# Kernel tuning notes

Measured on AMD Instinct MI355X. Metric: run time of the kernel, lower is better.

The kernel has to match this reference:

```python
import jax, jax.numpy as jnp
import numpy as np

N = 4096          # total ensemble boxes per frame
M = 20            # MAX_MERGE_NUMS
H = 16            # MergeNet hidden_c
COND_THRES = 0.2
IOU_THRES = 0.3


def setup_inputs() -> dict:
    key = jax.random.key(0)
    ks = jax.random.split(key, 6)
    u = jax.random.uniform(ks[0], (N, 9), dtype=jnp.float32)
    # realistic lidar boxes: centers in a ~140x80x8m range, dims in [0.5, 4.5), heading in [-pi, pi)
    centers = (u[:, 0:3] - 0.5) * jnp.array([140.0, 80.0, 8.0], jnp.float32)
    dims = u[:, 3:6] * 4.0 + 0.5
    heading = (u[:, 6:7] - 0.5) * (2.0 * np.pi)
    extra = u[:, 7:9]  # extra box attrs (cols 7:9), untouched by merge
    pred_boxes = jnp.concatenate([centers, dims, heading, extra], axis=-1)
    pred_scores = jax.random.uniform(ks[1], (N,), dtype=jnp.float32)
    pred_labels = jax.random.randint(ks[2], (N,), 0, 3)
    w1 = (jax.random.normal(ks[3], (M, H), jnp.float32) / np.sqrt(M)).astype(jnp.float32)
    b1 = jnp.zeros((H,), jnp.float32)
    w2 = (jax.random.normal(ks[4], (H, H), jnp.float32) / np.sqrt(H)).astype(jnp.float32)
    b2 = jnp.zeros((H,), jnp.float32)
    w3 = (jax.random.normal(ks[5], (H, 1), jnp.float32) / np.sqrt(H)).astype(jnp.float32)
    b3 = jnp.zeros((1,), jnp.float32)
    return dict(pred_boxes=pred_boxes, pred_scores=pred_scores, pred_labels=pred_labels,
                w1=w1, b1=b1, w2=w2, b2=b2, w3=w3, b3=b3)


def _bev_aligned(b):
    # boxes3d_lidar_to_aligned_bev_boxes: swap dx/dy when |limit_period(heading)| >= pi/4
    ang = b[..., 6] - jnp.floor(b[..., 6] / np.pi + 0.5) * np.pi
    swap = jnp.abs(ang) >= (np.pi / 4)
    dx = jnp.where(swap, b[..., 4], b[..., 3])
    dy = jnp.where(swap, b[..., 3], b[..., 4])
    return jnp.stack([b[..., 0] - dx / 2, b[..., 1] - dy / 2,
                      b[..., 0] + dx / 2, b[..., 1] + dy / 2], axis=-1)


def _iou_one_many(a, b):
    # axis-aligned BEV IoU of one box a[4] vs many b[N,4]
    xmin = jnp.maximum(a[0], b[:, 0]); ymin = jnp.maximum(a[1], b[:, 1])
    xmax = jnp.minimum(a[2], b[:, 2]); ymax = jnp.minimum(a[3], b[:, 3])
    inter = jnp.maximum(xmax - xmin, 0.0) * jnp.maximum(ymax - ymin, 0.0)
    area_a = (a[2] - a[0]) * (a[3] - a[1])
    area_b = (b[:, 2] - b[:, 0]) * (b[:, 3] - b[:, 1])
    return inter / jnp.maximum(area_a + area_b - inter, 1e-6)


def _nms_merge(pred_boxes, pred_scores, pred_labels, w1, b1, w2, b2, w3, b3):
    valid = pred_scores > COND_THRES
    sort_key = jnp.where(valid, pred_scores, -jnp.inf)
    order = jnp.argsort(-sort_key)                 # descending by score; invalid sink
    boxes9 = pred_boxes[order]
    labels = pred_labels[order]
    scores = pred_scores[order]
    suppressed0 = ~valid[order]
    boxes7 = boxes9[:, :7]
    bev0 = _bev_aligned(boxes7)                    # merged boxes get suppressed, so bev is static

    def mergenet(ob):                              # ob: [M, 7] -> merged box [7]
        x = ob.T                                   # [7, M] (k is the feature axis)
        h = jax.nn.relu(x @ w1 + b1)
        h = jax.nn.relu(h @ w2 + b2)
        return (h @ w3 + b3)[:, 0]

    def step(suppressed, i):
        active = ~suppressed[i]
        same = (labels == labels[i]) & (~suppressed)
        iou = _iou_one_many(bev0[i], bev0)         # [N]
        over = (iou > IOU_THRES) & same            # includes self (iou=1)
        count = jnp.sum(over)
        rank = jnp.cumsum(over) - 1                # slot of each overlap, in score order
        tgt = jnp.where(over & (rank < M), rank, M)
        ob = jnp.zeros((M, 7), boxes7.dtype).at[tgt].set(boxes7, mode='drop')
        bi = boxes7[i]
        new_box = jnp.where(count > 1, mergenet(ob), bi)
        new_box = new_box.at[3:6].set(jnp.maximum(new_box[3:6], 1e-5))
        out_box = jnp.where(active, new_box, bi)
        return suppressed | (over & active), (out_box, active)

    _, (merged7, keep) = jax.lax.scan(step, suppressed0, jnp.arange(N))
    out_boxes = jnp.concatenate([merged7, boxes9[:, 7:9]], axis=-1)   # [N, 9]
    return out_boxes, scores, labels, keep


def reference(pred_boxes, pred_scores, pred_labels, w1, b1, w2, b2, w3, b3):
    # Returns fixed-shape (boxes9, scores, labels, keep_mask); rows with keep=False
    # correspond to boxes that torch's dynamic version would have removed.
    return _nms_merge(pred_boxes, pred_scores, pred_labels, w1, b1, w2, b2, w3, b3)
```

## Files before the change

kernel.cpp:

```cpp
#include <hip/hip_runtime.h>
#include <cstdint>

typedef unsigned long long u64;
typedef unsigned int u32;

#define NB 4096
#define NW 64
#define MM 20
#define HH 16
#define COND_THRES 0.2f
#define IOU_THRES 0.3f
#define PI_F  3.14159265358979323846f
#define PI4_F 0.78539816339744830962f

#define WS_KEPT    0
#define WS_MASK    32768
#define WS_BOX9S   (WS_MASK + NB*NW*8)
#define WS_BEVS    (WS_BOX9S + NB*9*4)
#define WS_SCORES  (WS_BEVS + NB*16)
#define WS_LABELS  (WS_SCORES + NB*4)
#define WS_NBRW    (WS_LABELS + NB*4)
#define WS_PART    (WS_NBRW + NB*8)

__device__ __forceinline__ u64 sort_key(float s, int i) {
  u32 sb = (s > COND_THRES) ? __float_as_uint(s) : 0u;
  return ((u64)(sb ^ 0xFFFFFFFFu) << 12) | (u64)i;
}

__global__ void __launch_bounds__(256) k_rank(const float* __restrict__ scores,
                                              u32* __restrict__ partial,
                                              u64* __restrict__ nbrw) {
  __shared__ u64 kj[256];
  int tid = threadIdx.x;
  int j = blockIdx.y * 256 + tid;
  kj[tid] = sort_key(scores[j], j);
  __syncthreads();
  int i = blockIdx.x * 256 + tid;
  if (blockIdx.y == 0) nbrw[i] = 0;
  u64 ki = sort_key(scores[i], i);
  int cnt = 0;
  #pragma unroll 16
  for (int t = 0; t < 256; ++t) cnt += (kj[t] < ki) ? 1 : 0;
  partial[i * 16 + blockIdx.y] = (u32)cnt;
}

__global__ void __launch_bounds__(256) k_scatter(const u32* __restrict__ partial,
                                                 const float* __restrict__ scores,
                                                 const float* __restrict__ boxes9,
                                                 const int* __restrict__ labels,
                                                 float* __restrict__ box9s, float4* __restrict__ bevs,
                                                 float* __restrict__ scoress, int* __restrict__ labelss) {
  #pragma clang fp contract(off)
  int i = blockIdx.x * 256 + threadIdx.x;
  const uint4* p4 = (const uint4*)(partial + i * 16);
  uint4 a0 = p4[0], a1 = p4[1], a2 = p4[2], a3 = p4[3];
  int r = (int)(a0.x + a0.y + a0.z + a0.w + a1.x + a1.y + a1.z + a1.w +
                a2.x + a2.y + a2.z + a2.w + a3.x + a3.y + a3.z + a3.w);
  float b[9];
  #pragma unroll
  for (int f = 0; f < 9; ++f) b[f] = boxes9[i * 9 + f];
  #pragma unroll
  for (int f = 0; f < 9; ++f) box9s[r * 9 + f] = b[f];
  float ang = b[6] - floorf(b[6] / PI_F + 0.5f) * PI_F;
  bool sw = fabsf(ang) >= PI4_F;
  float dx = sw ? b[4] : b[3];
  float dy = sw ? b[3] : b[4];
  bevs[r] = make_float4(b[0] - dx * 0.5f, b[1] - dy * 0.5f,
                        b[0] + dx * 0.5f, b[1] + dy * 0.5f);
  scoress[r] = scores[i];
  labelss[r] = labels[i];
}

__global__ void __launch_bounds__(64) k_mask(const float4* __restrict__ bevs,
                                             const int* __restrict__ labelss,
                                             const float* __restrict__ scoress,
                                             u64* __restrict__ mask,
                                             u64* __restrict__ nbrw) {
  #pragma clang fp contract(off)
  __shared__ float4 bj[64];
  __shared__ int lj[64];
  int t = threadIdx.x;
  int jt = blockIdx.x;
  int it = blockIdx.y;
  int j = jt * 64 + t;
  bj[t] = bevs[j];
  lj[t] = labelss[j];
  u64 vj = __ballot(scoress[j] > COND_THRES);
  int i = it * 64 + t;
  float4 a = bevs[i];
  int la = labelss[i];
  float area_a = (a.z - a.x) * (a.w - a.y);
  __syncthreads();
  u64 w = 0;
  #pragma unroll 8
  for (int kk = 0; kk < 64; ++kk) {
    float4 bb = bj[kk];
    float xmin = fmaxf(a.x, bb.x), ymin = fmaxf(a.y, bb.y);
    float xmax = fminf(a.z, bb.z), ymax = fminf(a.w, bb.w);
    float inter = fmaxf(xmax - xmin, 0.0f) * fmaxf(ymax - ymin, 0.0f);
    float area_b = (bb.z - bb.x) * (bb.w - bb.y);
    float iou = inter / fmaxf(area_a + area_b - inter, 1e-6f);
    if ((iou > IOU_THRES) && (la == lj[kk])) w |= (1ull << kk);
  }
  mask[(u64)i * NW + jt] = w;
  if (jt <= it) {
    u64 below = (jt < it) ? ~0ull : ((1ull << t) - 1ull);
    if (w & vj & below) atomicOr(&nbrw[i], 1ull << jt);
  }
}

__global__ void __launch_bounds__(1024) k_nms(const u64* __restrict__ mask,
                                              const u64* __restrict__ nbrw,
                                              const float* __restrict__ scoress,
                                              u64* __restrict__ keptOut) {
  __shared__ u64 decided[64], kept[64];
  __shared__ int wavePending[16];
  __shared__ int anyPending;
  int tid = threadIdx.x;
  int lane = tid & 63;
  int waveId = tid >> 6;
  u64 dcache[4], kcache[4];
  #pragma unroll
  for (int s = 0; s < 4; ++s) {
    int i = tid + (s << 10);
    bool v = scoress[i] > COND_THRES;
    u64 vw = __ballot(v);
    dcache[s] = ~vw;
    kcache[s] = 0;
    if (lane == 0) {
      int wi = waveId + (s << 4);
      decided[wi] = ~vw;
      kept[wi] = 0;
    }
  }
  u64 cw0[4], cw1[4];
  u32 meta[4];
  #pragma unroll
  for (int s = 0; s < 4; ++s) {
    int i = tid + (s << 10);
    int wi = i >> 6;
    u64 bit = 1ull << (i & 63);
    u64 t = nbrw[i];
    int n = 0; u32 ovf = 0;
    u64 c0 = 0, c1 = 0; u32 i0 = 0, i1 = 0;
    while (t) {
      int w = __builtin_ctzll(t);
      t &= t - 1;
      u64 below = (w < wi) ? ~0ull : (bit - 1ull);
      u64 m = mask[(u64)i * NW + w] & below;
      if (n == 0)      { c0 = m; i0 = (u32)w; }
      else if (n == 1) { c1 = m; i1 = (u32)w; }
      else ovf = 1;
      ++n;
    }
    cw0[s] = c0; cw1[s] = c1;
    meta[s] = i0 | (i1 << 6) | ((u32)(n > 2 ? 2 : n) << 12) | (ovf << 14);
  }
  __syncthreads();
  while (true) {
    bool pend = false;
    #pragma unroll
    for (int s = 0; s < 4; ++s) {
      bool mine_und = !((dcache[s] >> lane) & 1ull);
      bool dec = false, keepme = false;
      if (mine_und) {
        bool hasU = false, hasK = false;
        u32 mt = meta[s];
        if (!(mt & (1u << 14))) {
          int n = (mt >> 12) & 3;
          if (n >= 1) {
            int w = mt & 63;
            u64 dw = decided[w], kw = kept[w];
            hasU = (cw0[s] & ~dw) != 0ull;
            hasK = (cw0[s] & kw) != 0ull;
          }
          if (n >= 2) {
            int w = (mt >> 6) & 63;
            u64 dw = decided[w], kw = kept[w];
            hasU = hasU || ((cw1[s] & ~dw) != 0ull);
            hasK = hasK || ((cw1[s] & kw) != 0ull);
          }
        } else {
          int i = tid + (s << 10);
          int wi = i >> 6;
          u64 bit = 1ull << (i & 63);
          u64 t = nbrw[i];
          while (t) {
            int w = __builtin_ctzll(t);
            t &= t - 1;
            u64 below = (w < wi) ? ~0ull : (bit - 1ull);
            u64 m = mask[(u64)i * NW + w] & below;
            hasU = hasU || ((m & ~decided[w]) != 0ull);
            hasK = hasK || ((m & kept[w]) != 0ull);
          }
        }
        dec = !hasU;
        keepme = !hasK;
      }
      u64 b_nd = __ballot(dec);
      u64 b_nk = __ballot(dec && keepme);
      dcache[s] |= b_nd;
      kcache[s] |= b_nk;
      pend |= (mine_und && !dec);
    }
    u64 pw = __ballot(pend);
    if (lane == 0) wavePending[waveId] = (pw != 0ull) ? 1 : 0;
    __syncthreads();
    if (lane == 0) {
      #pragma unroll
      for (int s = 0; s < 4; ++s) {
        int wi = waveId + (s << 4);
        decided[wi] = dcache[s];
        kept[wi] = kcache[s];
      }
    }
    if (tid == 0) {
      int any = 0;
      #pragma unroll
      for (int w = 0; w < 16; ++w) any |= wavePending[w];
      anyPending = any;
    }
    __syncthreads();
    if (!anyPending) break;
  }
  if (tid < 64) keptOut[tid] = kept[tid];
}

__global__ void __launch_bounds__(64) k_merge(
    const u64* __restrict__ mask, const u64* __restrict__ keptG,
    const float* __restrict__ box9s, const float* __restrict__ scoress,
    const int* __restrict__ labelss,
    const float* __restrict__ w1, const float* __restrict__ b1,
    const float* __restrict__ w2, const float* __restrict__ b2,
    const float* __restrict__ w3, const float* __restrict__ b3,
    float* __restrict__ out) {
  #pragma clang fp contract(off)
  __shared__ int candList[MM];
  __shared__ float ob[MM][7];
  __shared__ float h1[7][HH];
  __shared__ float h2[7][HH];
  __shared__ float res[7];
  __shared__ u64 K[64];
  int i = blockIdx.x;
  int t = threadIdx.x;
  K[t] = keptG[t];
  __syncthreads();
  bool active = (K[i >> 6] >> (i & 63)) & 1ull;
  u64 wq = 0;
  int cnt = 0;
  if (active) {
    u64 w = mask[(u64)i * NW + t];
    int hiw = i >> 6;
    u64 below = (1ull << (i & 63)) - 1ull;
    while (w) {
      int b = __builtin_ctzll(w);
      w &= w - 1;
      int j = (t << 6) | b;
      if (scoress[j] > COND_THRES) {
        const u64* rowj = mask + (u64)j * NW;
        u64 found = rowj[hiw] & K[hiw] & below;
        for (int ww = 0; ww < hiw; ++ww) found |= rowj[ww] & K[ww];
        if (!found) { wq |= (1ull << b); cnt++; }
      }
    }
  }
  int incl = cnt;
  #pragma unroll
  for (int off = 1; off < 64; off <<= 1) {
    int v = __shfl_up(incl, off);
    if (t >= off) incl += v;
  }
  int excl = incl - cnt;
  int count = __shfl(incl, 63);
  bool merged = active && (count > 1);
  if (merged && wq) {
    int pos = excl;
    u64 ww = wq;
    while (ww && pos < MM) {
      int b = __builtin_ctzll(ww);
      ww &= ww - 1;
      candList[pos++] = (t << 6) | b;
    }
  }
  __syncthreads();
  if (merged) {
    int nc = count < MM ? count : MM;
    if (t < MM) {
      if (t < nc) {
        int j = candList[t];
        #pragma unroll
        for (int f = 0; f < 7; ++f) ob[t][f] = box9s[j * 9 + f];
      } else {
        #pragma unroll
        for (int f = 0; f < 7; ++f) ob[t][f] = 0.0f;
      }
    }
    __syncthreads();
    for (int o = t; o < 7 * HH; o += 64) {
      int f = o >> 4, hh = o & 15;
      float acc = b1[hh];
      #pragma unroll
      for (int m = 0; m < MM; ++m) acc += ob[m][f] * w1[m * HH + hh];
      h1[f][hh] = fmaxf(acc, 0.0f);
    }
    __syncthreads();
    for (int o = t; o < 7 * HH; o += 64) {
      int f = o >> 4, oo = o & 15;
      float acc = b2[oo];
      #pragma unroll
      for (int k = 0; k < HH; ++k) acc += h1[f][k] * w2[k * HH + oo];
      h2[f][oo] = fmaxf(acc, 0.0f);
    }
    __syncthreads();
    if (t < 7) {
      float acc = b3[0];
      #pragma unroll
      for (int k = 0; k < HH; ++k) acc += h2[t][k] * w3[k];
      if (t >= 3 && t < 6) acc = fmaxf(acc, 1e-5f);
      res[t] = acc;
    }
    __syncthreads();
  }
  if (t < 9) {
    float v = box9s[i * 9 + t];
    if (merged && t < 7) v = res[t];
    out[i * 9 + t] = v;
  }
  if (t == 0) {
    out[NB * 9 + i]          = scoress[i];
    out[NB * 9 + NB + i]     = (float)labelss[i];
    out[NB * 9 + 2 * NB + i] = active ? 1.0f : 0.0f;
  }
}

extern "C" void kernel_launch(void* const* d_in, const int* in_sizes, int n_in,
                              void* d_out, int out_size, void* d_ws, size_t ws_size,
                              hipStream_t stream) {
  const float* boxes9 = (const float*)d_in[0];
  const float* scores = (const float*)d_in[1];
  const int*   labels = (const int*)d_in[2];
  const float* w1 = (const float*)d_in[3];
  const float* b1 = (const float*)d_in[4];
  const float* w2 = (const float*)d_in[5];
  const float* b2 = (const float*)d_in[6];
  const float* w3 = (const float*)d_in[7];
  const float* b3 = (const float*)d_in[8];
  char* ws = (char*)d_ws;
  u64*    kept    = (u64*)(ws + WS_KEPT);
  u64*    mask    = (u64*)(ws + WS_MASK);
  float*  box9s   = (float*)(ws + WS_BOX9S);
  float4* bevs    = (float4*)(ws + WS_BEVS);
  float*  scoress = (float*)(ws + WS_SCORES);
  int*    labelss = (int*)(ws + WS_LABELS);
  u64*    nbrw    = (u64*)(ws + WS_NBRW);
  u32*    part    = (u32*)(ws + WS_PART);
  float*  out     = (float*)d_out;

  hipLaunchKernelGGL(k_rank,    dim3(16, 16),   dim3(256),  0, stream, scores, part, nbrw);
  hipLaunchKernelGGL(k_scatter, dim3(NB / 256), dim3(256),  0, stream, part, scores, boxes9, labels,
                     box9s, bevs, scoress, labelss);
  hipLaunchKernelGGL(k_mask,    dim3(64, 64),   dim3(64),   0, stream, bevs, labelss, scoress,
                     mask, nbrw);
  hipLaunchKernelGGL(k_nms,     dim3(1),        dim3(1024), 0, stream, mask, nbrw, scoress, kept);
  hipLaunchKernelGGL(k_merge,   dim3(NB),       dim3(64),   0, stream, mask, kept,
                     box9s, scoress, labelss, w1, b1, w2, b2, w3, b3, out);
}
```

Baseline: 117.6 us.

## Fuse all five stages into one persistent kernel with atomic grid barriers

Replaces the five separate launches (rank, scatter, mask, nms, merge) with one 256-block by 1024-thread kernel whose stages are separated by a software grid barrier built on an atomic counter. Work is remapped so each wave handles one mask tile or one merge row, and the per-row merge scratch is carved from a shared memory pool. The aim is to remove the launch gaps and inter-kernel drain between stages. In exchange it needs all 256 blocks resident at once, adds a memset and spin-wait barriers, and runs the single-block NMS stage while the other blocks sit idle.

```diff
diff --git a/kernel.cpp b/kernel.cpp
--- a/kernel.cpp
+++ b/kernel.cpp
@@ -8,12 +8,14 @@
 #define NW 64
 #define MM 20
 #define HH 16
+#define GRID_BLOCKS 256
 #define COND_THRES 0.2f
 #define IOU_THRES 0.3f
 #define PI_F  3.14159265358979323846f
 #define PI4_F 0.78539816339744830962f
 
 #define WS_KEPT    0
+#define WS_CNT     1024
 #define WS_MASK    32768
 #define WS_BOX9S   (WS_MASK + NB*NW*8)
 #define WS_BEVS    (WS_BOX9S + NB*9*4)
@@ -27,309 +29,323 @@
   return ((u64)(sb ^ 0xFFFFFFFFu) << 12) | (u64)i;
 }
 
-__global__ void __launch_bounds__(256) k_rank(const float* __restrict__ scores,
-                                              u32* __restrict__ partial,
-                                              u64* __restrict__ nbrw) {
-  __shared__ u64 kj[256];
-  int tid = threadIdx.x;
-  int j = blockIdx.y * 256 + tid;
-  kj[tid] = sort_key(scores[j], j);
+__device__ __forceinline__ void grid_sync(u32* cnt, u32 target) {
   __syncthreads();
-  int i = blockIdx.x * 256 + tid;
-  if (blockIdx.y == 0) nbrw[i] = 0;
-  u64 ki = sort_key(scores[i], i);
-  int cnt = 0;
-  #pragma unroll 16
-  for (int t = 0; t < 256; ++t) cnt += (kj[t] < ki) ? 1 : 0;
-  partial[i * 16 + blockIdx.y] = (u32)cnt;
+  if (threadIdx.x == 0) {
+    __threadfence();
+    atomicAdd(cnt, 1u);
+    while (atomicAdd(cnt, 0u) < target) __builtin_amdgcn_s_sleep(2);
+  }
+  __syncthreads();
+  __threadfence();
 }
 
-__global__ void __launch_bounds__(256) k_scatter(const u32* __restrict__ partial,
-                                                 const float* __restrict__ scores,
-                                                 const float* __restrict__ boxes9,
-                                                 const int* __restrict__ labels,
-                                                 float* __restrict__ box9s, float4* __restrict__ bevs,
-                                                 float* __restrict__ scoress, int* __restrict__ labelss) {
-  #pragma clang fp contract(off)
-  int i = blockIdx.x * 256 + threadIdx.x;
-  const uint4* p4 = (const uint4*)(partial + i * 16);
-  uint4 a0 = p4[0], a1 = p4[1], a2 = p4[2], a3 = p4[3];
-  int r = (int)(a0.x + a0.y + a0.z + a0.w + a1.x + a1.y + a1.z + a1.w +
-                a2.x + a2.y + a2.z + a2.w + a3.x + a3.y + a3.z + a3.w);
-  float b[9];
-  #pragma unroll
-  for (int f = 0; f < 9; ++f) b[f] = boxes9[i * 9 + f];
-  #pragma unroll
-  for (int f = 0; f < 9; ++f) box9s[r * 9 + f] = b[f];
-  float ang = b[6] - floorf(b[6] / PI_F + 0.5f) * PI_F;
-  bool sw = fabsf(ang) >= PI4_F;
-  float dx = sw ? b[4] : b[3];
-  float dy = sw ? b[3] : b[4];
-  bevs[r] = make_float4(b[0] - dx * 0.5f, b[1] - dy * 0.5f,
-                        b[0] + dx * 0.5f, b[1] + dy * 0.5f);
-  scoress[r] = scores[i];
-  labelss[r] = labels[i];
-}
-
-__global__ void __launch_bounds__(64) k_mask(const float4* __restrict__ bevs,
-                                             const int* __restrict__ labelss,
-                                             const float* __restrict__ scoress,
-                                             u64* __restrict__ mask,
-                                             u64* __restrict__ nbrw) {
-  #pragma clang fp contract(off)
-  __shared__ float4 bj[64];
-  __shared__ int lj[64];
-  int t = threadIdx.x;
-  int jt = blockIdx.x;
-  int it = blockIdx.y;
-  int j = jt * 64 + t;
-  bj[t] = bevs[j];
-  lj[t] = labelss[j];
-  u64 vj = __ballot(scoress[j] > COND_THRES);
-  int i = it * 64 + t;
-  float4 a = bevs[i];
-  int la = labelss[i];
-  float area_a = (a.z - a.x) * (a.w - a.y);
-  __syncthreads();
-  u64 w = 0;
-  #pragma unroll 8
-  for (int kk = 0; kk < 64; ++kk) {
-    float4 bb = bj[kk];
-    float xmin = fmaxf(a.x, bb.x), ymin = fmaxf(a.y, bb.y);
-    float xmax = fminf(a.z, bb.z), ymax = fminf(a.w, bb.w);
-    float inter = fmaxf(xmax - xmin, 0.0f) * fmaxf(ymax - ymin, 0.0f);
-    float area_b = (bb.z - bb.x) * (bb.w - bb.y);
-    float iou = inter / fmaxf(area_a + area_b - inter, 1e-6f);
-    if ((iou > IOU_THRES) && (la == lj[kk])) w |= (1ull << kk);
-  }
-  mask[(u64)i * NW + jt] = w;
-  if (jt <= it) {
-    u64 below = (jt < it) ? ~0ull : ((1ull << t) - 1ull);
-    if (w & vj & below) atomicOr(&nbrw[i], 1ull << jt);
-  }
-}
-
-__global__ void __launch_bounds__(1024) k_nms(const u64* __restrict__ mask,
-                                              const u64* __restrict__ nbrw,
-                                              const float* __restrict__ scoress,
-                                              u64* __restrict__ keptOut) {
-  __shared__ u64 decided[64], kept[64];
-  __shared__ int wavePending[16];
-  __shared__ int anyPending;
-  int tid = threadIdx.x;
-  int lane = tid & 63;
-  int waveId = tid >> 6;
-  u64 dcache[4], kcache[4];
-  #pragma unroll
-  for (int s = 0; s < 4; ++s) {
-    int i = tid + (s << 10);
-    bool v = scoress[i] > COND_THRES;
-    u64 vw = __ballot(v);
-    dcache[s] = ~vw;
-    kcache[s] = 0;
-    if (lane == 0) {
-      int wi = waveId + (s << 4);
-      decided[wi] = ~vw;
-      kept[wi] = 0;
-    }
-  }
-  u64 cw0[4], cw1[4];
-  u32 meta[4];
-  #pragma unroll
-  for (int s = 0; s < 4; ++s) {
-    int i = tid + (s << 10);
-    int wi = i >> 6;
-    u64 bit = 1ull << (i & 63);
-    u64 t = nbrw[i];
-    int n = 0; u32 ovf = 0;
-    u64 c0 = 0, c1 = 0; u32 i0 = 0, i1 = 0;
-    while (t) {
-      int w = __builtin_ctzll(t);
-      t &= t - 1;
-      u64 below = (w < wi) ? ~0ull : (bit - 1ull);
-      u64 m = mask[(u64)i * NW + w] & below;
-      if (n == 0)      { c0 = m; i0 = (u32)w; }
-      else if (n == 1) { c1 = m; i1 = (u32)w; }
-      else ovf = 1;
-      ++n;
-    }
-    cw0[s] = c0; cw1[s] = c1;
-    meta[s] = i0 | (i1 << 6) | ((u32)(n > 2 ? 2 : n) << 12) | (ovf << 14);
-  }
-  __syncthreads();
-  while (true) {
-    bool pend = false;
-    #pragma unroll
-    for (int s = 0; s < 4; ++s) {
-      bool mine_und = !((dcache[s] >> lane) & 1ull);
-      bool dec = false, keepme = false;
-      if (mine_und) {
-        bool hasU = false, hasK = false;
-        u32 mt = meta[s];
-        if (!(mt & (1u << 14))) {
-          int n = (mt >> 12) & 3;
-          if (n >= 1) {
-            int w = mt & 63;
-            u64 dw = decided[w], kw = kept[w];
-            hasU = (cw0[s] & ~dw) != 0ull;
-            hasK = (cw0[s] & kw) != 0ull;
-          }
-          if (n >= 2) {
-            int w = (mt >> 6) & 63;
-            u64 dw = decided[w], kw = kept[w];
-            hasU = hasU || ((cw1[s] & ~dw) != 0ull);
-            hasK = hasK || ((cw1[s] & kw) != 0ull);
-          }
-        } else {
-          int i = tid + (s << 10);
-          int wi = i >> 6;
-          u64 bit = 1ull << (i & 63);
-          u64 t = nbrw[i];
-          while (t) {
-            int w = __builtin_ctzll(t);
-            t &= t - 1;
-            u64 below = (w < wi) ? ~0ull : (bit - 1ull);
-            u64 m = mask[(u64)i * NW + w] & below;
-            hasU = hasU || ((m & ~decided[w]) != 0ull);
-            hasK = hasK || ((m & kept[w]) != 0ull);
-          }
-        }
-        dec = !hasU;
-        keepme = !hasK;
-      }
-      u64 b_nd = __ballot(dec);
-      u64 b_nk = __ballot(dec && keepme);
-      dcache[s] |= b_nd;
-      kcache[s] |= b_nk;
-      pend |= (mine_und && !dec);
-    }
-    u64 pw = __ballot(pend);
-    if (lane == 0) wavePending[waveId] = (pw != 0ull) ? 1 : 0;
-    __syncthreads();
-    if (lane == 0) {
-      #pragma unroll
-      for (int s = 0; s < 4; ++s) {
-        int wi = waveId + (s << 4);
-        decided[wi] = dcache[s];
-        kept[wi] = kcache[s];
-      }
-    }
-    if (tid == 0) {
-      int any = 0;
-      #pragma unroll
-      for (int w = 0; w < 16; ++w) any |= wavePending[w];
-      anyPending = any;
-    }
-    __syncthreads();
-    if (!anyPending) break;
-  }
-  if (tid < 64) keptOut[tid] = kept[tid];
-}
-
-__global__ void __launch_bounds__(64) k_merge(
-    const u64* __restrict__ mask, const u64* __restrict__ keptG,
-    const float* __restrict__ box9s, const float* __restrict__ scoress,
-    const int* __restrict__ labelss,
+#define POOL_BYTES 25600
+
+__global__ void __launch_bounds__(1024) k_mega(
+    const float* __restrict__ boxes9, const float* __restrict__ scores,
+    const int* __restrict__ labels,
     const float* __restrict__ w1, const float* __restrict__ b1,
     const float* __restrict__ w2, const float* __restrict__ b2,
     const float* __restrict__ w3, const float* __restrict__ b3,
-    float* __restrict__ out) {
+    float* __restrict__ out,
+    u64* __restrict__ mask, float* __restrict__ box9s, float4* __restrict__ bevs,
+    float* __restrict__ scoress, int* __restrict__ labelss,
+    u64* __restrict__ nbrw, u32* __restrict__ partial,
+    u64* __restrict__ keptOut, u32* __restrict__ barCnt) {
   #pragma clang fp contract(off)
-  __shared__ int candList[MM];
-  __shared__ float ob[MM][7];
-  __shared__ float h1[7][HH];
-  __shared__ float h2[7][HH];
-  __shared__ float res[7];
-  __shared__ u64 K[64];
-  int i = blockIdx.x;
-  int t = threadIdx.x;
-  K[t] = keptG[t];
-  __syncthreads();
-  bool active = (K[i >> 6] >> (i & 63)) & 1ull;
-  u64 wq = 0;
-  int cnt = 0;
-  if (active) {
-    u64 w = mask[(u64)i * NW + t];
-    int hiw = i >> 6;
-    u64 below = (1ull << (i & 63)) - 1ull;
-    while (w) {
-      int b = __builtin_ctzll(w);
-      w &= w - 1;
-      int j = (t << 6) | b;
-      if (scoress[j] > COND_THRES) {
-        const u64* rowj = mask + (u64)j * NW;
-        u64 found = rowj[hiw] & K[hiw] & below;
-        for (int ww = 0; ww < hiw; ++ww) found |= rowj[ww] & K[ww];
-        if (!found) { wq |= (1ull << b); cnt++; }
-      }
-    }
-  }
-  int incl = cnt;
-  #pragma unroll
-  for (int off = 1; off < 64; off <<= 1) {
-    int v = __shfl_up(incl, off);
-    if (t >= off) incl += v;
-  }
-  int excl = incl - cnt;
-  int count = __shfl(incl, 63);
-  bool merged = active && (count > 1);
-  if (merged && wq) {
-    int pos = excl;
-    u64 ww = wq;
-    while (ww && pos < MM) {
-      int b = __builtin_ctzll(ww);
-      ww &= ww - 1;
-      candList[pos++] = (t << 6) | b;
-    }
-  }
-  __syncthreads();
-  if (merged) {
+  __shared__ __align__(16) char pool[POOL_BYTES];
+  __shared__ u64 nms_decided[64], nms_kept[64];
+  __shared__ int nms_wavePending[16];
+  __shared__ int nms_any;
+  const int tid = threadIdx.x;
+  const int bid = blockIdx.x;
+
+  {
+    u64* kj = (u64*)pool;
+    int bj = bid & 15, bi = bid >> 4;
+    if (tid < 256) kj[tid] = sort_key(scores[bj * 256 + tid], bj * 256 + tid);
+    __syncthreads();
+    if (tid < 256) {
+      int i = bi * 256 + tid;
+      if (bj == 0) nbrw[i] = 0;
+      u64 ki = sort_key(scores[i], i);
+      int c = 0;
+      #pragma unroll 16
+      for (int t2 = 0; t2 < 256; ++t2) c += (kj[t2] < ki) ? 1 : 0;
+      partial[i * 16 + bj] = (u32)c;
+    }
+  }
+  grid_sync(barCnt, 1 * GRID_BLOCKS);
+
+  if (bid < 4) {
+    int i = bid * 1024 + tid;
+    const uint4* p4 = (const uint4*)(partial + i * 16);
+    uint4 a0 = p4[0], a1 = p4[1], a2 = p4[2], a3 = p4[3];
+    int r = (int)(a0.x + a0.y + a0.z + a0.w + a1.x + a1.y + a1.z + a1.w +
+                  a2.x + a2.y + a2.z + a2.w + a3.x + a3.y + a3.z + a3.w);
+    float b[9];
+    #pragma unroll
+    for (int f = 0; f < 9; ++f) b[f] = boxes9[i * 9 + f];
+    #pragma unroll
+    for (int f = 0; f < 9; ++f) box9s[r * 9 + f] = b[f];
+    float ang = b[6] - floorf(b[6] / PI_F + 0.5f) * PI_F;
+    bool sw = fabsf(ang) >= PI4_F;
+    float dx = sw ? b[4] : b[3];
+    float dy = sw ? b[3] : b[4];
+    bevs[r] = make_float4(b[0] - dx * 0.5f, b[1] - dy * 0.5f,
+                          b[0] + dx * 0.5f, b[1] + dy * 0.5f);
+    scoress[r] = scores[i];
+    labelss[r] = labels[i];
+  }
+  grid_sync(barCnt, 2 * GRID_BLOCKS);
+
+  {
+    int waveId = tid >> 6;
+    int lane = tid & 63;
+    float4* bjW = ((float4*)pool) + waveId * 64;
+    int* ljW = ((int*)(pool + 16384)) + waveId * 64;
+    int wave = (bid << 4) | waveId;
+    int it = wave >> 6, jt = wave & 63;
+    int i = (it << 6) | lane;
+    int j = (jt << 6) | lane;
+    float4 a = bevs[i];
+    int la = labelss[i];
+    float area_a = (a.z - a.x) * (a.w - a.y);
+    bjW[lane] = bevs[j];
+    ljW[lane] = labelss[j];
+    u64 vj = __ballot(scoress[j] > COND_THRES);
+    __syncthreads();
+    u64 w = 0;
+    #pragma unroll 8
+    for (int kk = 0; kk < 64; ++kk) {
+      float4 bb = bjW[kk];
+      float xmin = fmaxf(a.x, bb.x), ymin = fmaxf(a.y, bb.y);
+      float xmax = fminf(a.z, bb.z), ymax = fminf(a.w, bb.w);
+      float inter = fmaxf(xmax - xmin, 0.0f) * fmaxf(ymax - ymin, 0.0f);
+      float area_b = (bb.z - bb.x) * (bb.w - bb.y);
+      float iou = inter / fmaxf(area_a + area_b - inter, 1e-6f);
+      if ((iou > IOU_THRES) && (la == ljW[kk])) w |= (1ull << kk);
+    }
+    mask[(u64)i * NW + jt] = w;
+    if (jt <= it) {
+      u64 below = (jt < it) ? ~0ull : ((1ull << lane) - 1ull);
+      if (w & vj & below) atomicOr(&nbrw[i], 1ull << jt);
+    }
+  }
+  grid_sync(barCnt, 3 * GRID_BLOCKS);
+
+  if (bid == 0) {
+    int lane = tid & 63;
+    int waveId = tid >> 6;
+    u64 dcache[4], kcache[4];
+    #pragma unroll
+    for (int s = 0; s < 4; ++s) {
+      int i = tid + (s << 10);
+      bool v = scoress[i] > COND_THRES;
+      u64 vw = __ballot(v);
+      dcache[s] = ~vw;
+      kcache[s] = 0;
+      if (lane == 0) {
+        int wi = waveId + (s << 4);
+        nms_decided[wi] = ~vw;
+        nms_kept[wi] = 0;
+      }
+    }
+    u64 cw0[4], cw1[4];
+    u32 meta[4];
+    #pragma unroll
+    for (int s = 0; s < 4; ++s) {
+      int i = tid + (s << 10);
+      int wi = i >> 6;
+      u64 bit = 1ull << (i & 63);
+      u64 t = nbrw[i];
+      int n = 0; u32 ovf = 0;
+      u64 c0 = 0, c1 = 0; u32 i0 = 0, i1 = 0;
+      while (t) {
+        int w = __builtin_ctzll(t);
+        t &= t - 1;
+        u64 below = (w < wi) ? ~0ull : (bit - 1ull);
+        u64 m = mask[(u64)i * NW + w] & below;
+        if (n == 0)      { c0 = m; i0 = (u32)w; }
+        else if (n == 1) { c1 = m; i1 = (u32)w; }
+        else ovf = 1;
+        ++n;
+      }
+      cw0[s] = c0; cw1[s] = c1;
+      meta[s] = i0 | (i1 << 6) | ((u32)(n > 2 ? 2 : n) << 12) | (ovf << 14);
+    }
+    __syncthreads();
+    while (true) {
+      bool pend = false;
+      #pragma unroll
+      for (int s = 0; s < 4; ++s) {
+        bool mine_und = !((dcache[s] >> lane) & 1ull);
+        bool dec = false, keepme = false;
+        if (mine_und) {
+          bool hasU = false, hasK = false;
+          u32 mt = meta[s];
+          if (!(mt & (1u << 14))) {
+            int n = (mt >> 12) & 3;
+            if (n >= 1) {
+              int w = mt & 63;
+              u64 dw = nms_decided[w], kw = nms_kept[w];
+              hasU = (cw0[s] & ~dw) != 0ull;
+              hasK = (cw0[s] & kw) != 0ull;
+            }
+            if (n >= 2) {
+              int w = (mt >> 6) & 63;
+              u64 dw = nms_decided[w], kw = nms_kept[w];
+              hasU = hasU || ((cw1[s] & ~dw) != 0ull);
+              hasK = hasK || ((cw1[s] & kw) != 0ull);
+            }
+          } else {
+            int i = tid + (s << 10);
+            int wi = i >> 6;
+            u64 bit = 1ull << (i & 63);
+            u64 t = nbrw[i];
+            while (t) {
+              int w = __builtin_ctzll(t);
+              t &= t - 1;
+              u64 below = (w < wi) ? ~0ull : (bit - 1ull);
+              u64 m = mask[(u64)i * NW + w] & below;
+              hasU = hasU || ((m & ~nms_decided[w]) != 0ull);
+              hasK = hasK || ((m & nms_kept[w]) != 0ull);
+            }
+          }
+          dec = !hasU;
+          keepme = !hasK;
+        }
+        u64 b_nd = __ballot(dec);
+        u64 b_nk = __ballot(dec && keepme);
+        dcache[s] |= b_nd;
+        kcache[s] |= b_nk;
+        pend |= (mine_und && !dec);
+      }
+      u64 pw = __ballot(pend);
+      if (lane == 0) nms_wavePending[waveId] = (pw != 0ull) ? 1 : 0;
+      __syncthreads();
+      if (lane == 0) {
+        #pragma unroll
+        for (int s = 0; s < 4; ++s) {
+          int wi = waveId + (s << 4);
+          nms_decided[wi] = dcache[s];
+          nms_kept[wi] = kcache[s];
+        }
+      }
+      if (tid == 0) {
+        int any = 0;
+        #pragma unroll
+        for (int w = 0; w < 16; ++w) any |= nms_wavePending[w];
+        nms_any = any;
+      }
+      __syncthreads();
+      if (!nms_any) break;
+    }
+    if (tid < 64) keptOut[tid] = nms_kept[tid];
+  }
+  grid_sync(barCnt, 4 * GRID_BLOCKS);
+
+  {
+    if (tid < 64) nms_kept[tid] = keptOut[tid];
+    __syncthreads();
+    int waveId = tid >> 6;
+    int lane = tid & 63;
+    int i = (bid << 4) | waveId;
+    char* ws5 = pool + waveId * 1600;
+    float (*ob)[7]  = (float(*)[7])(ws5);
+    float (*h1)[HH] = (float(*)[HH])(ws5 + 560);
+    float (*h2)[HH] = (float(*)[HH])(ws5 + 1008);
+    float* res      = (float*)(ws5 + 1456);
+    int* candList   = (int*)(ws5 + 1484);
+    bool active = (nms_kept[i >> 6] >> (i & 63)) & 1ull;
+    u64 wq = 0;
+    int cnt = 0;
+    if (active) {
+      u64 w = mask[(u64)i * NW + lane];
+      int hiw = i >> 6;
+      u64 below = (1ull << (i & 63)) - 1ull;
+      while (w) {
+        int b = __builtin_ctzll(w);
+        w &= w - 1;
+        int j = (lane << 6) | b;
+        if (scoress[j] > COND_THRES) {
+          const u64* rowj = mask + (u64)j * NW;
+          u64 found = rowj[hiw] & nms_kept[hiw] & below;
+          for (int ww = 0; ww < hiw; ++ww) found |= rowj[ww] & nms_kept[ww];
+          if (!found) { wq |= (1ull << b); cnt++; }
+        }
+      }
+    }
+    int incl = cnt;
+    #pragma unroll
+    for (int off = 1; off < 64; off <<= 1) {
+      int v = __shfl_up(incl, off);
+      if (lane >= off) incl += v;
+    }
+    int excl = incl - cnt;
+    int count = __shfl(incl, 63);
+    bool merged = active && (count > 1);
+    if (merged && wq) {
+      int pos = excl;
+      u64 ww = wq;
+      while (ww && pos < MM) {
+        int b = __builtin_ctzll(ww);
+        ww &= ww - 1;
+        candList[pos++] = (lane << 6) | b;
+      }
+    }
+    __syncthreads();
     int nc = count < MM ? count : MM;
-    if (t < MM) {
-      if (t < nc) {
-        int j = candList[t];
-        #pragma unroll
-        for (int f = 0; f < 7; ++f) ob[t][f] = box9s[j * 9 + f];
+    if (merged && lane < MM) {
+      if (lane < nc) {
+        int j = candList[lane];
+        #pragma unroll
+        for (int f = 0; f < 7; ++f) ob[lane][f] = box9s[j * 9 + f];
       } else {
         #pragma unroll
-        for (int f = 0; f < 7; ++f) ob[t][f] = 0.0f;
-      }
-    }
-    __syncthreads();
-    for (int o = t; o < 7 * HH; o += 64) {
-      int f = o >> 4, hh = o & 15;
-      float acc = b1[hh];
-      #pragma unroll
-      for (int m = 0; m < MM; ++m) acc += ob[m][f] * w1[m * HH + hh];
-      h1[f][hh] = fmaxf(acc, 0.0f);
-    }
-    __syncthreads();
-    for (int o = t; o < 7 * HH; o += 64) {
-      int f = o >> 4, oo = o & 15;
-      float acc = b2[oo];
-      #pragma unroll
-      for (int k = 0; k < HH; ++k) acc += h1[f][k] * w2[k * HH + oo];
-      h2[f][oo] = fmaxf(acc, 0.0f);
-    }
-    __syncthreads();
-    if (t < 7) {
+        for (int f = 0; f < 7; ++f) ob[lane][f] = 0.0f;
+      }
+    }
+    __syncthreads();
+    if (merged) {
+      for (int o = lane; o < 7 * HH; o += 64) {
+        int f = o >> 4, hh = o & 15;
+        float acc = b1[hh];
+        #pragma unroll
+        for (int m = 0; m < MM; ++m) acc += ob[m][f] * w1[m * HH + hh];
+        h1[f][hh] = fmaxf(acc, 0.0f);
+      }
+    }
+    __syncthreads();
+    if (merged) {
+      for (int o = lane; o < 7 * HH; o += 64) {
+        int f = o >> 4, oo = o & 15;
+        float acc = b2[oo];
+        #pragma unroll
+        for (int k = 0; k < HH; ++k) acc += h1[f][k] * w2[k * HH + oo];
+        h2[f][oo] = fmaxf(acc, 0.0f);
+      }
+    }
+    __syncthreads();
+    if (merged && lane < 7) {
       float acc = b3[0];
       #pragma unroll
-      for (int k = 0; k < HH; ++k) acc += h2[t][k] * w3[k];
-      if (t >= 3 && t < 6) acc = fmaxf(acc, 1e-5f);
-      res[t] = acc;
-    }
-    __syncthreads();
-  }
-  if (t < 9) {
-    float v = box9s[i * 9 + t];
-    if (merged && t < 7) v = res[t];
-    out[i * 9 + t] = v;
-  }
-  if (t == 0) {
-    out[NB * 9 + i]          = scoress[i];
-    out[NB * 9 + NB + i]     = (float)labelss[i];
-    out[NB * 9 + 2 * NB + i] = active ? 1.0f : 0.0f;
+      for (int k = 0; k < HH; ++k) acc += h2[lane][k] * w3[k];
+      if (lane >= 3 && lane < 6) acc = fmaxf(acc, 1e-5f);
+      res[lane] = acc;
+    }
+    __syncthreads();
+    if (lane < 9) {
+      float v = box9s[i * 9 + lane];
+      if (merged && lane < 7) v = res[lane];
+      out[i * 9 + lane] = v;
+    }
+    if (lane == 0) {
+      out[NB * 9 + i]          = scoress[i];
+      out[NB * 9 + NB + i]     = (float)labelss[i];
+      out[NB * 9 + 2 * NB + i] = active ? 1.0f : 0.0f;
+    }
   }
 }
 
@@ -354,14 +370,11 @@
   int*    labelss = (int*)(ws + WS_LABELS);
   u64*    nbrw    = (u64*)(ws + WS_NBRW);
   u32*    part    = (u32*)(ws + WS_PART);
+  u32*    barCnt  = (u32*)(ws + WS_CNT);
   float*  out     = (float*)d_out;
 
-  hipLaunchKernelGGL(k_rank,    dim3(16, 16),   dim3(256),  0, stream, scores, part, nbrw);
-  hipLaunchKernelGGL(k_scatter, dim3(NB / 256), dim3(256),  0, stream, part, scores, boxes9, labels,
-                     box9s, bevs, scoress, labelss);
-  hipLaunchKernelGGL(k_mask,    dim3(64, 64),   dim3(64),   0, stream, bevs, labelss, scoress,
-                     mask, nbrw);
-  hipLaunchKernelGGL(k_nms,     dim3(1),        dim3(1024), 0, stream, mask, nbrw, scoress, kept);
-  hipLaunchKernelGGL(k_merge,   dim3(NB),       dim3(64),   0, stream, mask, kept,
-                     box9s, scoress, labelss, w1, b1, w2, b2, w3, b3, out);
+  hipMemsetAsync(barCnt, 0, sizeof(u32), stream);
+  hipLaunchKernelGGL(k_mega, dim3(GRID_BLOCKS), dim3(1024), 0, stream,
+                     boxes9, scores, labels, w1, b1, w2, b2, w3, b3, out,
+                     mask, box9s, bevs, scoress, labelss, nbrw, part, kept, barCnt);
 }
```

Result: slower. 410.4 us (+249.0%).

## Fuse rank and scatter kernels; resolve NMS word-by-word in one wavefront

Applied to the files above, without the earlier changes.

The rank and scatter kernels are merged into one prep kernel. Each block loads all sort keys into shared memory, computes ranks for 16 boxes, and scatters them directly, which drops one launch and the global partial-count buffer. The NMS kernel no longer iterates block-wide fixpoint rounds with __syncthreads. It precomputes per-box intra-word and cross-word masks into shared memory, then a single wavefront walks the 64 words in order, using shuffles to fetch already-final kept words and a ballot loop to resolve dependencies inside each word. This trades block-level barrier iterations for a serial 64-step chain on one wave, plus larger shared memory use.

```diff
diff --git a/kernel.cpp b/kernel.cpp
--- a/kernel.cpp
+++ b/kernel.cpp
@@ -20,55 +20,52 @@
 #define WS_SCORES  (WS_BEVS + NB*16)
 #define WS_LABELS  (WS_SCORES + NB*4)
 #define WS_NBRW    (WS_LABELS + NB*4)
-#define WS_PART    (WS_NBRW + NB*8)
 
 __device__ __forceinline__ u64 sort_key(float s, int i) {
   u32 sb = (s > COND_THRES) ? __float_as_uint(s) : 0u;
   return ((u64)(sb ^ 0xFFFFFFFFu) << 12) | (u64)i;
 }
 
-__global__ void __launch_bounds__(256) k_rank(const float* __restrict__ scores,
-                                              u32* __restrict__ partial,
+__global__ void __launch_bounds__(256) k_prep(const float* __restrict__ scores,
+                                              const float* __restrict__ boxes9,
+                                              const int* __restrict__ labels,
+                                              float* __restrict__ box9s, float4* __restrict__ bevs,
+                                              float* __restrict__ scoress, int* __restrict__ labelss,
                                               u64* __restrict__ nbrw) {
-  __shared__ u64 kj[256];
+  #pragma clang fp contract(off)
+  __shared__ u64 keys[NB];
+  __shared__ u32 part[16][16];
   int tid = threadIdx.x;
-  int j = blockIdx.y * 256 + tid;
-  kj[tid] = sort_key(scores[j], j);
-  __syncthreads();
-  int i = blockIdx.x * 256 + tid;
-  if (blockIdx.y == 0) nbrw[i] = 0;
-  u64 ki = sort_key(scores[i], i);
-  int cnt = 0;
+  for (int k = tid; k < NB; k += 256) keys[k] = sort_key(scores[k], k);
+  __syncthreads();
+  int bl = tid & 15;
+  int ch = tid >> 4;
+  u64 ki = keys[blockIdx.x * 16 + bl];
+  int c = 0;
   #pragma unroll 16
-  for (int t = 0; t < 256; ++t) cnt += (kj[t] < ki) ? 1 : 0;
-  partial[i * 16 + blockIdx.y] = (u32)cnt;
-}
-
-__global__ void __launch_bounds__(256) k_scatter(const u32* __restrict__ partial,
-                                                 const float* __restrict__ scores,
-                                                 const float* __restrict__ boxes9,
-                                                 const int* __restrict__ labels,
-                                                 float* __restrict__ box9s, float4* __restrict__ bevs,
-                                                 float* __restrict__ scoress, int* __restrict__ labelss) {
-  #pragma clang fp contract(off)
-  int i = blockIdx.x * 256 + threadIdx.x;
-  const uint4* p4 = (const uint4*)(partial + i * 16);
-  uint4 a0 = p4[0], a1 = p4[1], a2 = p4[2], a3 = p4[3];
-  int r = (int)(a0.x + a0.y + a0.z + a0.w + a1.x + a1.y + a1.z + a1.w +
-                a2.x + a2.y + a2.z + a2.w + a3.x + a3.y + a3.z + a3.w);
-  float b[9];
-  #pragma unroll
-  for (int f = 0; f < 9; ++f) b[f] = boxes9[i * 9 + f];
-  #pragma unroll
-  for (int f = 0; f < 9; ++f) box9s[r * 9 + f] = b[f];
-  float ang = b[6] - floorf(b[6] / PI_F + 0.5f) * PI_F;
-  bool sw = fabsf(ang) >= PI4_F;
-  float dx = sw ? b[4] : b[3];
-  float dy = sw ? b[3] : b[4];
-  bevs[r] = make_float4(b[0] - dx * 0.5f, b[1] - dy * 0.5f,
-                        b[0] + dx * 0.5f, b[1] + dy * 0.5f);
-  scoress[r] = scores[i];
-  labelss[r] = labels[i];
+  for (int t = 0; t < 256; ++t) c += (keys[(ch << 8) + t] < ki) ? 1 : 0;
+  part[bl][ch] = (u32)c;
+  __syncthreads();
+  if (tid < 16) {
+    int i = blockIdx.x * 16 + tid;
+    int r = 0;
+    #pragma unroll
+    for (int q = 0; q < 16; ++q) r += (int)part[tid][q];
+    nbrw[i] = 0;
+    float b[9];
+    #pragma unroll
+    for (int f = 0; f < 9; ++f) b[f] = boxes9[i * 9 + f];
+    #pragma unroll
+    for (int f = 0; f < 9; ++f) box9s[r * 9 + f] = b[f];
+    float ang = b[6] - floorf(b[6] / PI_F + 0.5f) * PI_F;
+    bool sw = fabsf(ang) >= PI4_F;
+    float dx = sw ? b[4] : b[3];
+    float dy = sw ? b[3] : b[4];
+    bevs[r] = make_float4(b[0] - dx * 0.5f, b[1] - dy * 0.5f,
+                          b[0] + dx * 0.5f, b[1] + dy * 0.5f);
+    scoress[r] = scores[i];
+    labelss[r] = labels[i];
+  }
 }
 
 __global__ void __launch_bounds__(64) k_mask(const float4* __restrict__ bevs,
@@ -113,117 +110,89 @@
                                               const u64* __restrict__ nbrw,
                                               const float* __restrict__ scoress,
                                               u64* __restrict__ keptOut) {
-  __shared__ u64 decided[64], kept[64];
-  __shared__ int wavePending[16];
-  __shared__ int anyPending;
+  __shared__ u64 csL[NB];
+  __shared__ u64 ce0L[NB];
+  __shared__ u64 ce1L[NB];
+  __shared__ u64 remL[NB];
+  __shared__ u32 emL[NB];
+  __shared__ u64 vwL[64];
   int tid = threadIdx.x;
   int lane = tid & 63;
   int waveId = tid >> 6;
-  u64 dcache[4], kcache[4];
   #pragma unroll
-  for (int s = 0; s < 4; ++s) {
-    int i = tid + (s << 10);
+  for (int s4 = 0; s4 < 4; ++s4) {
+    int i = tid + (s4 << 10);
     bool v = scoress[i] > COND_THRES;
-    u64 vw = __ballot(v);
-    dcache[s] = ~vw;
-    kcache[s] = 0;
-    if (lane == 0) {
-      int wi = waveId + (s << 4);
-      decided[wi] = ~vw;
-      kept[wi] = 0;
-    }
-  }
-  u64 cw0[4], cw1[4];
-  u32 meta[4];
+    u64 vb = __ballot(v);
+    if (lane == 0) vwL[waveId + (s4 << 4)] = vb;
+  }
   #pragma unroll
-  for (int s = 0; s < 4; ++s) {
-    int i = tid + (s << 10);
+  for (int s4 = 0; s4 < 4; ++s4) {
+    int i = tid + (s4 << 10);
     int wi = i >> 6;
     u64 bit = 1ull << (i & 63);
     u64 t = nbrw[i];
-    int n = 0; u32 ovf = 0;
-    u64 c0 = 0, c1 = 0; u32 i0 = 0, i1 = 0;
+    u64 cs = 0, c0 = 0, c1 = 0, rem = 0;
+    u32 i0 = 0, i1 = 0; int n = 0;
     while (t) {
       int w = __builtin_ctzll(t);
       t &= t - 1;
-      u64 below = (w < wi) ? ~0ull : (bit - 1ull);
-      u64 m = mask[(u64)i * NW + w] & below;
-      if (n == 0)      { c0 = m; i0 = (u32)w; }
-      else if (n == 1) { c1 = m; i1 = (u32)w; }
-      else ovf = 1;
-      ++n;
-    }
-    cw0[s] = c0; cw1[s] = c1;
-    meta[s] = i0 | (i1 << 6) | ((u32)(n > 2 ? 2 : n) << 12) | (ovf << 14);
-  }
-  __syncthreads();
-  while (true) {
-    bool pend = false;
-    #pragma unroll
-    for (int s = 0; s < 4; ++s) {
-      bool mine_und = !((dcache[s] >> lane) & 1ull);
-      bool dec = false, keepme = false;
-      if (mine_und) {
-        bool hasU = false, hasK = false;
-        u32 mt = meta[s];
-        if (!(mt & (1u << 14))) {
-          int n = (mt >> 12) & 3;
-          if (n >= 1) {
-            int w = mt & 63;
-            u64 dw = decided[w], kw = kept[w];
-            hasU = (cw0[s] & ~dw) != 0ull;
-            hasK = (cw0[s] & kw) != 0ull;
-          }
-          if (n >= 2) {
-            int w = (mt >> 6) & 63;
-            u64 dw = decided[w], kw = kept[w];
-            hasU = hasU || ((cw1[s] & ~dw) != 0ull);
-            hasK = hasK || ((cw1[s] & kw) != 0ull);
-          }
-        } else {
-          int i = tid + (s << 10);
-          int wi = i >> 6;
-          u64 bit = 1ull << (i & 63);
-          u64 t = nbrw[i];
-          while (t) {
-            int w = __builtin_ctzll(t);
-            t &= t - 1;
-            u64 below = (w < wi) ? ~0ull : (bit - 1ull);
-            u64 m = mask[(u64)i * NW + w] & below;
-            hasU = hasU || ((m & ~decided[w]) != 0ull);
-            hasK = hasK || ((m & kept[w]) != 0ull);
-          }
+      u64 m = mask[(u64)i * NW + w];
+      if (w == wi) {
+        cs = m & (bit - 1ull);
+      } else {
+        if (n == 0)      { c0 = m; i0 = (u32)w; }
+        else if (n == 1) { c1 = m; i1 = (u32)w; }
+        else rem |= 1ull << w;
+        ++n;
+      }
+    }
+    csL[i] = cs; ce0L[i] = c0; ce1L[i] = c1; remL[i] = rem;
+    emL[i] = i0 | (i1 << 6);
+  }
+  __syncthreads();
+  if (tid < 64) {
+    u64 keptW = 0;
+    u64 cs_c = csL[lane], ce0_c = ce0L[lane], ce1_c = ce1L[lane], rem_c = remL[lane];
+    u32 em_c = emL[lane];
+    u64 vws_c = vwL[0];
+    for (int s = 0; s < 64; ++s) {
+      u64 cs_n = 0, ce0_n = 0, ce1_n = 0, rem_n = 0, vws_n = 0; u32 em_n = 0;
+      if (s < 63) {
+        int ip = ((s + 1) << 6) | lane;
+        cs_n = csL[ip]; ce0_n = ce0L[ip]; ce1_n = ce1L[ip];
+        rem_n = remL[ip]; em_n = emL[ip]; vws_n = vwL[s + 1];
+      }
+      int w0 = (int)(em_c & 63u), w1 = (int)((em_c >> 6) & 63u);
+      u64 k0 = __shfl(keptW, w0);
+      u64 k1 = __shfl(keptW, w1);
+      bool hk = ((ce0_c & k0) | (ce1_c & k1)) != 0ull;
+      u64 rem = rem_c;
+      while (__ballot(rem != 0ull) != 0ull) {
+        int w = rem ? __builtin_ctzll(rem) : 0;
+        u64 kws = __shfl(keptW, w);
+        if (rem) {
+          u64 m = mask[(u64)((s << 6) | lane) * NW + w];
+          hk = hk || ((m & kws) != 0ull);
+          rem &= rem - 1;
         }
-        dec = !hasU;
-        keepme = !hasK;
-      }
-      u64 b_nd = __ballot(dec);
-      u64 b_nk = __ballot(dec && keepme);
-      dcache[s] |= b_nd;
-      kcache[s] |= b_nk;
-      pend |= (mine_und && !dec);
-    }
-    u64 pw = __ballot(pend);
-    if (lane == 0) wavePending[waveId] = (pw != 0ull) ? 1 : 0;
-    __syncthreads();
-    if (lane == 0) {
-      #pragma unroll
-      for (int s = 0; s < 4; ++s) {
-        int wi = waveId + (s << 4);
-        decided[wi] = dcache[s];
-        kept[wi] = kcache[s];
-      }
-    }
-    if (tid == 0) {
-      int any = 0;
-      #pragma unroll
-      for (int w = 0; w < 16; ++w) any |= wavePending[w];
-      anyPending = any;
-    }
-    __syncthreads();
-    if (!anyPending) break;
-  }
-  if (tid < 64) keptOut[tid] = kept[tid];
+      }
+      u64 dw = ~vws_c;
+      u64 kw = 0;
+      bool und = (vws_c >> lane) & 1ull;
+      while (true) {
+        bool dec = und && ((cs_c & ~dw) == 0ull);
+        bool keep = dec && !hk && ((cs_c & kw) == 0ull);
+        dw |= __ballot(dec);
+        kw |= __ballot(keep);
+        und = und && !dec;
+        if (__ballot(und) == 0ull) break;
+      }
+      if (lane == s) keptW = kw;
+      cs_c = cs_n; ce0_c = ce0_n; ce1_c = ce1_n; rem_c = rem_n; em_c = em_n; vws_c = vws_n;
+    }
+    keptOut[lane] = keptW;
+  }
 }
 
 __global__ void __launch_bounds__(64) k_merge(
@@ -353,15 +322,15 @@
   float*  scoress = (float*)(ws + WS_SCORES);
   int*    labelss = (int*)(ws + WS_LABELS);
   u64*    nbrw    = (u64*)(ws + WS_NBRW);
-  u32*    part    = (u32*)(ws + WS_PART);
   float*  out     = (float*)d_out;
 
-  hipLaunchKernelGGL(k_rank,    dim3(16, 16),   dim3(256),  0, stream, scores, part, nbrw);
-  hipLaunchKernelGGL(k_scatter, dim3(NB / 256), dim3(256),  0, stream, part, scores, boxes9, labels,
-                     box9s, bevs, scoress, labelss);
-  hipLaunchKernelGGL(k_mask,    dim3(64, 64),   dim3(64),   0, stream, bevs, labelss, scoress,
-                     mask, nbrw);
-  hipLaunchKernelGGL(k_nms,     dim3(1),        dim3(1024), 0, stream, mask, nbrw, scoress, kept);
-  hipLaunchKernelGGL(k_merge,   dim3(NB),       dim3(64),   0, stream, mask, kept,
-                     box9s, scoress, labelss, w1, b1, w2, b2, w3, b3, out);
-}
+  hipLaunchKernelGGL(k_prep,  dim3(256),    dim3(256),  0, stream,
+                     scores, boxes9, labels, box9s, bevs, scoress, labelss, nbrw);
+  hipLaunchKernelGGL(k_mask,  dim3(64, 64), dim3(64),   0, stream,
+                     bevs, labelss, scoress, mask, nbrw);
+  hipLaunchKernelGGL(k_nms,   dim3(1),      dim3(1024), 0, stream,
+                     mask, nbrw, scoress, kept);
+  hipLaunchKernelGGL(k_merge, dim3(NB),     dim3(64),   0, stream,
+                     mask, kept, box9s, scoress, labelss,
+                     w1, b1, w2, b2, w3, b3, out);
+}
```

Measured after the change: 131.3 us. 1.12x slower.

## Fuse rank and scatter kernels; compute only lower-triangle IoU mask and transpose

Applied to the files above, without the earlier changes.

Merges the rank-counting and scatter kernels into one kernel that loads all sort keys into shared memory and reduces the partial counts there, dropping a launch and the global partial buffer. The mask kernel now skips upper-triangle tiles and fills them by transposing the lower-triangle bit tiles through shared memory, using the symmetry of IoU and label equality. This halves the IoU computation at the cost of extra stores and a shuffle. The fused prep kernel has only 16 active threads doing the scatter per block, and each block recomputes all keys.

```diff
diff --git a/kernel.cpp b/kernel.cpp
--- a/kernel.cpp
+++ b/kernel.cpp
@@ -20,55 +20,52 @@
 #define WS_SCORES  (WS_BEVS + NB*16)
 #define WS_LABELS  (WS_SCORES + NB*4)
 #define WS_NBRW    (WS_LABELS + NB*4)
-#define WS_PART    (WS_NBRW + NB*8)
 
 __device__ __forceinline__ u64 sort_key(float s, int i) {
   u32 sb = (s > COND_THRES) ? __float_as_uint(s) : 0u;
   return ((u64)(sb ^ 0xFFFFFFFFu) << 12) | (u64)i;
 }
 
-__global__ void __launch_bounds__(256) k_rank(const float* __restrict__ scores,
-                                              u32* __restrict__ partial,
+__global__ void __launch_bounds__(256) k_prep(const float* __restrict__ scores,
+                                              const float* __restrict__ boxes9,
+                                              const int* __restrict__ labels,
+                                              float* __restrict__ box9s, float4* __restrict__ bevs,
+                                              float* __restrict__ scoress, int* __restrict__ labelss,
                                               u64* __restrict__ nbrw) {
-  __shared__ u64 kj[256];
+  #pragma clang fp contract(off)
+  __shared__ u64 keys[NB];
+  __shared__ u32 part[16][16];
   int tid = threadIdx.x;
-  int j = blockIdx.y * 256 + tid;
-  kj[tid] = sort_key(scores[j], j);
-  __syncthreads();
-  int i = blockIdx.x * 256 + tid;
-  if (blockIdx.y == 0) nbrw[i] = 0;
-  u64 ki = sort_key(scores[i], i);
-  int cnt = 0;
+  for (int k = tid; k < NB; k += 256) keys[k] = sort_key(scores[k], k);
+  __syncthreads();
+  int bl = tid & 15;
+  int ch = tid >> 4;
+  u64 ki = keys[blockIdx.x * 16 + bl];
+  int c = 0;
   #pragma unroll 16
-  for (int t = 0; t < 256; ++t) cnt += (kj[t] < ki) ? 1 : 0;
-  partial[i * 16 + blockIdx.y] = (u32)cnt;
-}
-
-__global__ void __launch_bounds__(256) k_scatter(const u32* __restrict__ partial,
-                                                 const float* __restrict__ scores,
-                                                 const float* __restrict__ boxes9,
-                                                 const int* __restrict__ labels,
-                                                 float* __restrict__ box9s, float4* __restrict__ bevs,
-                                                 float* __restrict__ scoress, int* __restrict__ labelss) {
-  #pragma clang fp contract(off)
-  int i = blockIdx.x * 256 + threadIdx.x;
-  const uint4* p4 = (const uint4*)(partial + i * 16);
-  uint4 a0 = p4[0], a1 = p4[1], a2 = p4[2], a3 = p4[3];
-  int r = (int)(a0.x + a0.y + a0.z + a0.w + a1.x + a1.y + a1.z + a1.w +
-                a2.x + a2.y + a2.z + a2.w + a3.x + a3.y + a3.z + a3.w);
-  float b[9];
-  #pragma unroll
-  for (int f = 0; f < 9; ++f) b[f] = boxes9[i * 9 + f];
-  #pragma unroll
-  for (int f = 0; f < 9; ++f) box9s[r * 9 + f] = b[f];
-  float ang = b[6] - floorf(b[6] / PI_F + 0.5f) * PI_F;
-  bool sw = fabsf(ang) >= PI4_F;
-  float dx = sw ? b[4] : b[3];
-  float dy = sw ? b[3] : b[4];
-  bevs[r] = make_float4(b[0] - dx * 0.5f, b[1] - dy * 0.5f,
-                        b[0] + dx * 0.5f, b[1] + dy * 0.5f);
-  scoress[r] = scores[i];
-  labelss[r] = labels[i];
+  for (int t = 0; t < 256; ++t) c += (keys[(ch << 8) + t] < ki) ? 1 : 0;
+  part[bl][ch] = (u32)c;
+  __syncthreads();
+  if (tid < 16) {
+    int i = blockIdx.x * 16 + tid;
+    int r = 0;
+    #pragma unroll
+    for (int q = 0; q < 16; ++q) r += (int)part[tid][q];
+    nbrw[i] = 0;
+    float b[9];
+    #pragma unroll
+    for (int f = 0; f < 9; ++f) b[f] = boxes9[i * 9 + f];
+    #pragma unroll
+    for (int f = 0; f < 9; ++f) box9s[r * 9 + f] = b[f];
+    float ang = b[6] - floorf(b[6] / PI_F + 0.5f) * PI_F;
+    bool sw = fabsf(ang) >= PI4_F;
+    float dx = sw ? b[4] : b[3];
+    float dy = sw ? b[3] : b[4];
+    bevs[r] = make_float4(b[0] - dx * 0.5f, b[1] - dy * 0.5f,
+                          b[0] + dx * 0.5f, b[1] + dy * 0.5f);
+    scoress[r] = scores[i];
+    labelss[r] = labels[i];
+  }
 }
 
 __global__ void __launch_bounds__(64) k_mask(const float4* __restrict__ bevs,
@@ -79,9 +76,11 @@
   #pragma clang fp contract(off)
   __shared__ float4 bj[64];
   __shared__ int lj[64];
+  __shared__ u64 tw[64];
   int t = threadIdx.x;
   int jt = blockIdx.x;
   int it = blockIdx.y;
+  if (jt > it) return;
   int j = jt * 64 + t;
   bj[t] = bevs[j];
   lj[t] = labelss[j];
@@ -103,9 +102,17 @@
     if ((iou > IOU_THRES) && (la == lj[kk])) w |= (1ull << kk);
   }
   mask[(u64)i * NW + jt] = w;
-  if (jt <= it) {
+  {
     u64 below = (jt < it) ? ~0ull : ((1ull << t) - 1ull);
     if (w & vj & below) atomicOr(&nbrw[i], 1ull << jt);
+  }
+  if (jt < it) {
+    tw[t] = w;
+    __syncthreads();
+    u64 wT = 0;
+    #pragma unroll 8
+    for (int k = 0; k < 64; ++k) wT |= ((tw[k] >> t) & 1ull) << k;
+    mask[(u64)j * NW + it] = wT;
   }
 }
 
@@ -353,15 +360,15 @@
   float*  scoress = (float*)(ws + WS_SCORES);
   int*    labelss = (int*)(ws + WS_LABELS);
   u64*    nbrw    = (u64*)(ws + WS_NBRW);
-  u32*    part    = (u32*)(ws + WS_PART);
   float*  out     = (float*)d_out;
 
-  hipLaunchKernelGGL(k_rank,    dim3(16, 16),   dim3(256),  0, stream, scores, part, nbrw);
-  hipLaunchKernelGGL(k_scatter, dim3(NB / 256), dim3(256),  0, stream, part, scores, boxes9, labels,
-                     box9s, bevs, scoress, labelss);
-  hipLaunchKernelGGL(k_mask,    dim3(64, 64),   dim3(64),   0, stream, bevs, labelss, scoress,
-                     mask, nbrw);
-  hipLaunchKernelGGL(k_nms,     dim3(1),        dim3(1024), 0, stream, mask, nbrw, scoress, kept);
-  hipLaunchKernelGGL(k_merge,   dim3(NB),       dim3(64),   0, stream, mask, kept,
-                     box9s, scoress, labelss, w1, b1, w2, b2, w3, b3, out);
-}
+  hipLaunchKernelGGL(k_prep,  dim3(256),    dim3(256),  0, stream,
+                     scores, boxes9, labels, box9s, bevs, scoress, labelss, nbrw);
+  hipLaunchKernelGGL(k_mask,  dim3(64, 64), dim3(64),   0, stream,
+                     bevs, labelss, scoress, mask, nbrw);
+  hipLaunchKernelGGL(k_nms,   dim3(1),      dim3(1024), 0, stream,
+                     mask, nbrw, scoress, kept);
+  hipLaunchKernelGGL(k_merge, dim3(NB),     dim3(64),   0, stream,
+                     mask, kept, box9s, scoress, labelss,
+                     w1, b1, w2, b2, w3, b3, out);
+}
```

New measurement: 119.6 us. Within noise of the previous version (+1.7%).
